# Kernel tuning notes

Hardware: AMD Instinct MI355X
Metric: run time of the kernel (lower is better)

The kernel has to match this reference:

```python
import jax, jax.numpy as jnp
import numpy as np

N = 25000          # nodes
E = 200000         # edges
MUL = 16           # multiplicity of 0e and 1o in irreps_in/out
NUM_RADIAL = 8
HIDDEN = 64
WNUMEL = 4 * MUL * MUL
PATH_ALPHA = 1.0 / np.sqrt(2.0 * MUL)   # 2 paths feed each output irrep, fan_in=MUL each
INV_SQRT3 = 1.0 / np.sqrt(3.0)          # CG coeff for 1o x 1o -> 0e (component norm)


def setup_inputs() -> dict:
    key = jax.random.key(0)
    ks = jax.random.split(key, 9)
    x = jax.random.normal(ks[0], (N, 4 * MUL), jnp.float32)          # [N, 64] = 16x0e + 16x1o
    edge_attr = jax.random.normal(ks[1], (E, 4), jnp.float32)        # [E, 4]  = 1x0e + 1x1o sh
    edge_length = jax.random.uniform(ks[2], (E,), jnp.float32, 0.0, 5.0)
    edge_src = jax.random.randint(ks[3], (E,), 0, N)
    edge_dst = jax.random.randint(ks[4], (E,), 0, N)
    W1 = jax.random.normal(ks[5], (NUM_RADIAL, HIDDEN), jnp.float32)
    W2 = jax.random.normal(ks[6], (HIDDEN, WNUMEL), jnp.float32)
    L0 = jax.random.normal(ks[7], (MUL, MUL), jnp.float32)           # sc Linear on 0e block
    L1 = jax.random.normal(ks[8], (MUL, MUL), jnp.float32)           # sc Linear on 1o block
    return dict(x=x, edge_attr=edge_attr, edge_length=edge_length,
                edge_src=edge_src, edge_dst=edge_dst, W1=W1, W2=W2, L0=L0, L1=L1)


def reference(x, edge_attr, edge_length, edge_src, edge_dst, W1, W2, L0, L1):
    # ---- radial Gaussian basis (centers linspace(0,5,8), sigma=1) ----
    centers = jnp.linspace(0.0, 5.0, NUM_RADIAL).astype(x.dtype)
    d = edge_length[:, None] - centers[None, :]
    radial = jnp.exp(-0.5 * d * d)                                   # [E, 8]
    # ---- radial MLP -> per-edge TP weights (e3nn FullyConnectedNet, silu) ----
    h = jax.nn.silu(radial @ W1 * (1.0 / np.sqrt(NUM_RADIAL)))       # [E, 64]
    w = (h @ W2 * (1.0 / np.sqrt(HIDDEN))).reshape(E, 4, MUL, MUL)   # [E, 4, 16, 16]
    # ---- gather source node features, split into l=0 and l=1 parts ----
    xj = x[edge_src]                                                  # [E, 64]
    xj0 = xj[:, :MUL]                                                 # [E, 16]
    xj1 = xj[:, MUL:].reshape(E, MUL, 3)                              # [E, 16, 3]
    sh0 = edge_attr[:, 0]                                             # [E]
    sh1 = edge_attr[:, 1:4]                                           # [E, 3]
    # ---- FullyConnectedTensorProduct: 4 CG paths with per-edge weights ----
    m0 = (jnp.einsum('eu,euv->ev', xj0 * sh0[:, None], w[:, 0])
          + INV_SQRT3 * jnp.einsum('euk,ek,euv->ev', xj1, sh1, w[:, 1])) * PATH_ALPHA  # [E,16]
    m1 = (jnp.einsum('eu,ek,euv->evk', xj0, sh1, w[:, 2])
          + jnp.einsum('euk,e,euv->evk', xj1, sh0, w[:, 3])) * PATH_ALPHA              # [E,16,3]
    m_ij = jnp.concatenate([m0, m1.reshape(E, 3 * MUL)], axis=1)      # [E, 64]
    # ---- scatter-add messages to destination nodes ----
    m_i = jax.ops.segment_sum(m_ij, edge_dst, num_segments=N)        # [N, 64]
    # ---- residual self-connection: o3.Linear per-l mixing ----
    x0 = x[:, :MUL]
    x1 = x[:, MUL:].reshape(N, MUL, 3)
    sc0 = x0 @ L0
    sc1 = jnp.einsum('nuk,uv->nvk', x1, L1).reshape(N, 3 * MUL)
    sc = jnp.concatenate([sc0, sc1], axis=1) * (1.0 / np.sqrt(MUL))
    return m_i + sc
```

## Files before the change

### kernel.cpp

```cpp
#include <hip/hip_runtime.h>

#define N_NODES 25000
#define N_EDGES 200000

constexpr int ET = 32;
constexpr int NTILES = 6250;
constexpr int GRID = 512;
constexpr int XPS = 584;
constexpr int XRS = 18;
constexpr int CTS = 36;

typedef __attribute__((ext_vector_type(8))) _Float16 half8;
typedef __attribute__((ext_vector_type(4))) _Float16 half4;
typedef __attribute__((ext_vector_type(4))) float float4v;

__device__ __forceinline__ void gl_lds16(const void* g, void* l) {
    __builtin_amdgcn_global_load_lds((const __attribute__((address_space(1))) void*)g,
                                     (__attribute__((address_space(3))) void*)l, 16, 0, 0);
}
__device__ __forceinline__ void gl_lds4(const void* g, void* l) {
    __builtin_amdgcn_global_load_lds((const __attribute__((address_space(1))) void*)g,
                                     (__attribute__((address_space(3))) void*)l, 4, 0, 0);
}

__global__ __launch_bounds__(512, 4) void fused_kernel(
    const float* __restrict__ x, const float* __restrict__ edge_attr,
    const float* __restrict__ edge_length, const int* __restrict__ edge_src,
    const int* __restrict__ edge_dst, const float* __restrict__ W1,
    const float* __restrict__ W2, const float* __restrict__ L0,
    const float* __restrict__ L1, float* __restrict__ out) {

    const int t = threadIdx.x;
    const int w = t >> 6;
    const int lane = t & 63;
    const int q = w >> 1;
    const int uh = w & 1;
    const int qm = t & 15;
    const int quad = (t >> 4) & 3;
    const int eL = t >> 4;
    const int uL = t & 15;
    const int uS = (uL + ((eL & 3) << 2)) & 15;

    __shared__ __attribute__((aligned(16))) _Float16 lds_h16[ET * 72];
    __shared__ __attribute__((aligned(16))) float lds_cfT[3][16][CTS];
    __shared__ __attribute__((aligned(16))) float lds_cf3T[3][16][CTS];
    __shared__ __attribute__((aligned(16))) float lds_xch[12 * XPS];
    __shared__ __attribute__((aligned(16))) float lds_w1t[64 * 8];
    __shared__ __attribute__((aligned(16))) float l0[256], l1[256];
    __shared__ __attribute__((aligned(16))) float lds_xj[3][ET * 64];
    __shared__ __attribute__((aligned(16))) float lds_ea[3][ET * 4];
    __shared__ __attribute__((aligned(16))) float lds_len[3][ET];
    __shared__ __attribute__((aligned(16))) int   lds_dst[3][ET];
    __shared__ __attribute__((aligned(16))) int   lds_srcb[3][ET];

    half8 bfr[8][2];
    {
        float scale = 0.0220970869f;
        if (q == 1) scale *= 0.5773502692f;
        const int kr = quad * 8;
        #pragma unroll
        for (int up = 0; up < 8; ++up) {
            const int col = q * 256 + (uh * 8 + up) * 16 + qm;
            #pragma unroll
            for (int kf = 0; kf < 2; ++kf) {
                half8 f;
                #pragma unroll
                for (int j = 0; j < 8; ++j) {
                    const int k = kf * 32 + kr + j;
                    f[j] = (_Float16)(W2[k * 1024 + col] * scale);
                }
                bfr[up][kf] = f;
            }
        }
    }
    lds_w1t[(t & 63) * 8 + (t >> 6)] = W1[t];
    if (t < 256) l0[t] = L0[t];
    else         l1[t - 256] = L1[t - 256];

    int T = blockIdx.x;
    if (w == 0 && lane < ET) gl_lds4(edge_src + T * ET + lane, &lds_srcb[0][0]);
    if (w == 1 && lane < ET) gl_lds4(edge_src + (T + GRID) * ET + lane, &lds_srcb[1][0]);
    if (w == 2 && lane < ET) gl_lds4(edge_src + (T + 2 * GRID) * ET + lane, &lds_srcb[2][0]);
    __syncthreads();
    {
        const int e4 = (w << 2) + (lane >> 4);
        const int c4 = (lane & 15) * 4;
        gl_lds16(x + lds_srcb[0][e4] * 64 + c4, &lds_xj[0][w * 256]);
        gl_lds16(x + lds_srcb[1][e4] * 64 + c4, &lds_xj[1][w * 256]);
    }
    if (w == 0 && lane < ET) gl_lds16(edge_attr + 4 * (T * ET + lane), &lds_ea[0][0]);
    if (w == 1 && lane < ET) gl_lds4(edge_length + T * ET + lane, &lds_len[0][0]);
    if (w == 2 && lane < ET) gl_lds4(edge_dst + T * ET + lane, &lds_dst[0][0]);
    if (w == 3 && lane < ET) gl_lds16(edge_attr + 4 * ((T + GRID) * ET + lane), &lds_ea[1][0]);
    if (w == 4 && lane < ET) gl_lds4(edge_length + (T + GRID) * ET + lane, &lds_len[1][0]);
    if (w == 5 && lane < ET) gl_lds4(edge_dst + (T + GRID) * ET + lane, &lds_dst[1][0]);

    {
        const bool is0 = lane < 16;
        const int qq = lane - 16;
        const int v = is0 ? lane : qq / 3;
        const int k = is0 ? 0 : qq - 3 * v;
        const float* mat = is0 ? l0 : l1;
        for (int n = blockIdx.x * 8 + w; n < N_NODES; n += GRID * 8) {
            const float xv = x[n * 64 + lane];
            float s = 0.f;
            #pragma unroll
            for (int u = 0; u < 16; ++u) {
                const int sel = is0 ? u : 16 + 3 * u + k;
                s = fmaf(__shfl(xv, sel), mat[u * 16 + v], s);
            }
            atomicAdd(out + n * 64 + lane, 0.25f * s);
        }
    }
    __syncthreads();

    int p = 0;
    while (true) {
        {
            const float sh0 = lds_ea[p][eL * 4 + 0];
            const float s1x = lds_ea[p][eL * 4 + 1];
            const float s1y = lds_ea[p][eL * 4 + 2];
            const float s1z = lds_ea[p][eL * 4 + 3];
            const float* xr = &lds_xj[p][eL * 64];
            const float xj0v = xr[uS];
            const float x0 = xr[16 + 3 * uS];
            const float x1 = xr[17 + 3 * uS];
            const float x2 = xr[18 + 3 * uS];
            lds_cfT[0][uS][eL] = xj0v * sh0;
            lds_cfT[1][uS][eL] = fmaf(x0, s1x, fmaf(x1, s1y, x2 * s1z));
            lds_cfT[2][uS][eL] = xj0v;
            lds_cf3T[0][uS][eL] = x0 * sh0;
            lds_cf3T[1][uS][eL] = x1 * sh0;
            lds_cf3T[2][uS][eL] = x2 * sh0;
            const int c0 = uS * 4;
            const float len = lds_len[p][eL];
            float rad[8];
            #pragma unroll
            for (int r = 0; r < 8; ++r) {
                const float d = len - 0.7142857143f * (float)r;
                rad[r] = __expf(-0.5f * d * d);
            }
            half4 hv;
            #pragma unroll
            for (int i = 0; i < 4; ++i) {
                const float4v wA = *(const float4v*)(&lds_w1t[(c0 + i) * 8]);
                const float4v wB = *(const float4v*)(&lds_w1t[(c0 + i) * 8 + 4]);
                float s = rad[0] * wA[0] + rad[1] * wA[1] + rad[2] * wA[2] + rad[3] * wA[3]
                        + rad[4] * wB[0] + rad[5] * wB[1] + rad[6] * wB[2] + rad[7] * wB[3];
                s *= 0.3535533906f;
                hv[i] = (_Float16)(s / (1.f + __expf(-s)));
            }
            *(half4*)(&lds_h16[eL * 72 + c0]) = hv;
        }

        __syncthreads();

        const int T2 = T + 2 * GRID;
        if (T2 < NTILES) {
            const int p2 = (p + 2) % 3;
            {
                const int e4 = (w << 2) + (lane >> 4);
                const int src = lds_srcb[p2][e4];
                gl_lds16(x + src * 64 + (lane & 15) * 4, &lds_xj[p2][w * 256]);
            }
            if (w == 0 && lane < ET) gl_lds16(edge_attr + 4 * (T2 * ET + lane), &lds_ea[p2][0]);
            if (w == 1 && lane < ET) gl_lds4(edge_length + T2 * ET + lane, &lds_len[p2][0]);
            if (w == 2 && lane < ET) gl_lds4(edge_dst + T2 * ET + lane, &lds_dst[p2][0]);
            if (w == 3 && lane < ET) {
                const int e3 = min((T + 3 * GRID) * ET + lane, N_EDGES - 1);
                gl_lds4(edge_src + e3, &lds_srcb[p][0]);
            }
        }

        if (q < 3) {
            #pragma unroll
            for (int mt = 0; mt < 2; ++mt) {
                const half8 a0 = *(const half8*)(&lds_h16[(mt * 16 + qm) * 72 + quad * 8]);
                const half8 a1 = *(const half8*)(&lds_h16[(mt * 16 + qm) * 72 + 32 + quad * 8]);
                float4v C = (float4v){0.f, 0.f, 0.f, 0.f};
                #pragma unroll
                for (int up = 0; up < 8; ++up) {
                    const int u = uh * 8 + up;
                    float4v au = __builtin_amdgcn_mfma_f32_16x16x32_f16(
                        a0, bfr[up][0], (float4v){0.f, 0.f, 0.f, 0.f}, 0, 0, 0);
                    au = __builtin_amdgcn_mfma_f32_16x16x32_f16(a1, bfr[up][1], au, 0, 0, 0);
                    const float4v cr = *(const float4v*)(&lds_cfT[q][u][mt * 16 + quad * 4]);
                    C += au * cr;
                }
                float* xb = &lds_xch[(q * 2 + uh) * XPS];
                #pragma unroll
                for (int r = 0; r < 4; ++r)
                    xb[(mt * 16 + quad * 4 + r) * XRS + qm] = C[r];
            }
        } else {
            #pragma unroll
            for (int mt = 0; mt < 2; ++mt) {
                const half8 a0 = *(const half8*)(&lds_h16[(mt * 16 + qm) * 72 + quad * 8]);
                const half8 a1 = *(const half8*)(&lds_h16[(mt * 16 + qm) * 72 + 32 + quad * 8]);
                float4v C3[3];
                C3[0] = (float4v){0.f, 0.f, 0.f, 0.f};
                C3[1] = (float4v){0.f, 0.f, 0.f, 0.f};
                C3[2] = (float4v){0.f, 0.f, 0.f, 0.f};
                #pragma unroll
                for (int up = 0; up < 8; ++up) {
                    const int u = uh * 8 + up;
                    float4v au = __builtin_amdgcn_mfma_f32_16x16x32_f16(
                        a0, bfr[up][0], (float4v){0.f, 0.f, 0.f, 0.f}, 0, 0, 0);
                    au = __builtin_amdgcn_mfma_f32_16x16x32_f16(a1, bfr[up][1], au, 0, 0, 0);
                    #pragma unroll
                    for (int k = 0; k < 3; ++k) {
                        const float4v ck = *(const float4v*)(&lds_cf3T[k][u][mt * 16 + quad * 4]);
                        C3[k] += au * ck;
                    }
                }
                #pragma unroll
                for (int k = 0; k < 3; ++k) {
                    float* xb = &lds_xch[(6 + uh * 3 + k) * XPS];
                    #pragma unroll
                    for (int r = 0; r < 4; ++r)
                        xb[(mt * 16 + quad * 4 + r) * XRS + qm] = C3[k][r];
                }
            }
        }

        __syncthreads();

        #pragma unroll
        for (int i = 0; i < 4; ++i) {
            const int idx = t + 512 * i;
            const int e = idx >> 6, j = idx & 63;
            float val;
            if (j < 16) {
                val = (lds_xch[0 * XPS + e * XRS + j] + lds_xch[1 * XPS + e * XRS + j])
                    + (lds_xch[2 * XPS + e * XRS + j] + lds_xch[3 * XPS + e * XRS + j]);
            } else {
                const int qj = j - 16, v = qj / 3, k = qj - 3 * v;
                const float s2 = lds_xch[4 * XPS + e * XRS + v] + lds_xch[5 * XPS + e * XRS + v];
                const float s3 = lds_xch[(6 + k) * XPS + e * XRS + v]
                               + lds_xch[(9 + k) * XPS + e * XRS + v];
                val = fmaf(s2, lds_ea[p][e * 4 + 1 + k], s3);
            }
            atomicAdd(out + lds_dst[p][e] * 64 + j, val);
        }

        const int Tn = T + GRID;
        if (Tn >= NTILES) break;
        T = Tn;
        p = (p + 1) % 3;
    }
}

extern "C" void kernel_launch(void* const* d_in, const int* in_sizes, int n_in,
                              void* d_out, int out_size, void* d_ws, size_t ws_size,
                              hipStream_t stream) {
    const float* x           = (const float*)d_in[0];
    const float* edge_attr   = (const float*)d_in[1];
    const float* edge_length = (const float*)d_in[2];
    const int*   edge_src    = (const int*)d_in[3];
    const int*   edge_dst    = (const int*)d_in[4];
    const float* W1          = (const float*)d_in[5];
    const float* W2          = (const float*)d_in[6];
    const float* L0          = (const float*)d_in[7];
    const float* L1          = (const float*)d_in[8];
    float* out = (float*)d_out;

    hipMemsetAsync(out, 0, (size_t)N_NODES * 64 * sizeof(float), stream);
    fused_kernel<<<GRID, 512, 0, stream>>>(
        x, edge_attr, edge_length, edge_src, edge_dst, W1, W2, L0, L1, out);
}
```

Before: 181.5 us.

## Issue next-tile prefetch before coefficient stage and use lighter LDS-only barrier

```diff
diff --git a/kernel.cpp b/kernel.cpp
--- a/kernel.cpp
+++ b/kernel.cpp
@@ -21,6 +21,12 @@
 __device__ __forceinline__ void gl_lds4(const void* g, void* l) {
     __builtin_amdgcn_global_load_lds((const __attribute__((address_space(1))) void*)g,
                                      (__attribute__((address_space(3))) void*)l, 4, 0, 0);
+}
+
+__device__ __forceinline__ void wg_barrier() {
+    asm volatile("s_waitcnt lgkmcnt(0)" ::: "memory");
+    __builtin_amdgcn_s_barrier();
+    asm volatile("" ::: "memory");
 }
 
 __global__ __launch_bounds__(512, 4) void fused_kernel(
@@ -48,10 +54,10 @@
     __shared__ __attribute__((aligned(16))) float lds_w1t[64 * 8];
     __shared__ __attribute__((aligned(16))) float l0[256], l1[256];
     __shared__ __attribute__((aligned(16))) float lds_xj[3][ET * 64];
-    __shared__ __attribute__((aligned(16))) float lds_ea[3][ET * 4];
-    __shared__ __attribute__((aligned(16))) float lds_len[3][ET];
-    __shared__ __attribute__((aligned(16))) int   lds_dst[3][ET];
-    __shared__ __attribute__((aligned(16))) int   lds_srcb[3][ET];
+    __shared__ __attribute__((aligned(16))) float lds_ea[4][ET * 4];
+    __shared__ __attribute__((aligned(16))) float lds_len[4][ET];
+    __shared__ __attribute__((aligned(16))) int   lds_dst[4][ET];
+    __shared__ __attribute__((aligned(16))) int   lds_srcb[4][ET];
 
     half8 bfr[8][2];
     {
@@ -115,12 +121,31 @@
     __syncthreads();
 
     int p = 0;
+    int m = 0;
     while (true) {
+        const int T2 = T + 2 * GRID;
+        if (T2 < NTILES) {
+            const int p2 = (p < 1) ? p + 2 : p - 1;
+            const int m2 = (m + 2) & 3;
+            {
+                const int e4 = (w << 2) + (lane >> 4);
+                const int src = lds_srcb[m2][e4];
+                gl_lds16(x + src * 64 + (lane & 15) * 4, &lds_xj[p2][w * 256]);
+            }
+            if (w == 0 && lane < ET) gl_lds16(edge_attr + 4 * (T2 * ET + lane), &lds_ea[m2][0]);
+            if (w == 1 && lane < ET) gl_lds4(edge_length + T2 * ET + lane, &lds_len[m2][0]);
+            if (w == 2 && lane < ET) gl_lds4(edge_dst + T2 * ET + lane, &lds_dst[m2][0]);
+            if (w == 3 && lane < ET) {
+                const int e3 = min((T + 3 * GRID) * ET + lane, N_EDGES - 1);
+                gl_lds4(edge_src + e3, &lds_srcb[(m + 3) & 3][0]);
+            }
+        }
+
         {
-            const float sh0 = lds_ea[p][eL * 4 + 0];
-            const float s1x = lds_ea[p][eL * 4 + 1];
-            const float s1y = lds_ea[p][eL * 4 + 2];
-            const float s1z = lds_ea[p][eL * 4 + 3];
+            const float sh0 = lds_ea[m][eL * 4 + 0];
+            const float s1x = lds_ea[m][eL * 4 + 1];
+            const float s1y = lds_ea[m][eL * 4 + 2];
+            const float s1z = lds_ea[m][eL * 4 + 3];
             const float* xr = &lds_xj[p][eL * 64];
             const float xj0v = xr[uS];
             const float x0 = xr[16 + 3 * uS];
@@ -133,7 +158,7 @@
             lds_cf3T[1][uS][eL] = x1 * sh0;
             lds_cf3T[2][uS][eL] = x2 * sh0;
             const int c0 = uS * 4;
-            const float len = lds_len[p][eL];
+            const float len = lds_len[m][eL];
             float rad[8];
             #pragma unroll
             for (int r = 0; r < 8; ++r) {
@@ -153,24 +178,7 @@
             *(half4*)(&lds_h16[eL * 72 + c0]) = hv;
         }
 
-        __syncthreads();
-
-        const int T2 = T + 2 * GRID;
-        if (T2 < NTILES) {
-            const int p2 = (p + 2) % 3;
-            {
-                const int e4 = (w << 2) + (lane >> 4);
-                const int src = lds_srcb[p2][e4];
-                gl_lds16(x + src * 64 + (lane & 15) * 4, &lds_xj[p2][w * 256]);
-            }
-            if (w == 0 && lane < ET) gl_lds16(edge_attr + 4 * (T2 * ET + lane), &lds_ea[p2][0]);
-            if (w == 1 && lane < ET) gl_lds4(edge_length + T2 * ET + lane, &lds_len[p2][0]);
-            if (w == 2 && lane < ET) gl_lds4(edge_dst + T2 * ET + lane, &lds_dst[p2][0]);
-            if (w == 3 && lane < ET) {
-                const int e3 = min((T + 3 * GRID) * ET + lane, N_EDGES - 1);
-                gl_lds4(edge_src + e3, &lds_srcb[p][0]);
-            }
-        }
+        wg_barrier();
 
         if (q < 3) {
             #pragma unroll
@@ -238,15 +246,15 @@
                 const float s2 = lds_xch[4 * XPS + e * XRS + v] + lds_xch[5 * XPS + e * XRS + v];
                 const float s3 = lds_xch[(6 + k) * XPS + e * XRS + v]
                                + lds_xch[(9 + k) * XPS + e * XRS + v];
-                val = fmaf(s2, lds_ea[p][e * 4 + 1 + k], s3);
-            }
-            atomicAdd(out + lds_dst[p][e] * 64 + j, val);
-        }
-
-        const int Tn = T + GRID;
-        if (Tn >= NTILES) break;
-        T = Tn;
-        p = (p + 1) % 3;
+                val = fmaf(s2, lds_ea[m][e * 4 + 1 + k], s3);
+            }
+            atomicAdd(out + lds_dst[m][e] * 64 + j, val);
+        }
+
+        T += GRID;
+        if (T >= NTILES) break;
+        p = (p < 2) ? p + 1 : 0;
+        m = (m + 1) & 3;
     }
 }
 
```

After: 180.9 us, median of 2. About the same (-0.4%).
